# Performance work log

Measured on AMD Instinct MI355X. Metric: run time of the kernel, lower is better.

## Reference

```python
import jax, jax.numpy as jnp
import numpy as np

D_MODEL = 1024
N_HEADS = 16
D_K = D_MODEL // N_HEADS


def setup_inputs() -> dict:
    key = jax.random.key(0)
    k1, k2, k3 = jax.random.split(key, 3)
    x = jax.random.normal(k1, (4, 2048, D_MODEL), dtype=jnp.float32)
    # torch nn.Linear(d, 3d, bias=False): y = x @ W.T ; we store W.T directly as (in, out)
    w_qkv = jax.random.normal(k2, (D_MODEL, 3 * D_MODEL), dtype=jnp.float32) * (1.0 / np.sqrt(D_MODEL))
    w_out = jax.random.normal(k3, (D_MODEL, D_MODEL), dtype=jnp.float32) * (1.0 / np.sqrt(D_MODEL))
    return {"x": x, "w_qkv": w_qkv, "w_out": w_out}


def reference(x, w_qkv, w_out):
    B, T, D = x.shape
    qkv = jnp.einsum('btd,de->bte', x, w_qkv)  # (B,T,3D)
    q, k, v = jnp.split(qkv, 3, axis=-1)
    # split heads -> (B,H,T,d_k)
    def split_heads(t):
        return t.reshape(B, T, N_HEADS, D_K).transpose(0, 2, 1, 3)
    q, k, v = split_heads(q), split_heads(k), split_heads(v)
    scale = 1.0 / np.sqrt(D_K).astype(np.float32)
    scores = jnp.einsum('bhqd,bhkd->bhqk', q, k) * scale  # (B,H,T,T)
    causal = jnp.triu(jnp.full((T, T), -jnp.inf, dtype=scores.dtype), k=1)
    scores = scores + causal[None, None]
    weights = jax.nn.softmax(scores, axis=-1)
    attn = jnp.einsum('bhqk,bhkd->bhqd', weights, v)
    attn = attn.transpose(0, 2, 1, 3).reshape(B, T, D)
    return jnp.einsum('btd,de->bte', attn, w_out)
```

## Files before the change

kernel.cpp:

```cpp
#include <hip/hip_runtime.h>
#include <hip/hip_bf16.h>

typedef short short8 __attribute__((ext_vector_type(8)));
typedef float f32x4 __attribute__((ext_vector_type(4)));

#define MFMA16(a, b, c) __builtin_amdgcn_mfma_f32_16x16x32_bf16((a), (b), (c), 0, 0, 0)

#define GLOAD16(gp, lp)                                                    \
    __builtin_amdgcn_global_load_lds(                                      \
        (const __attribute__((address_space(1))) unsigned int*)(gp),       \
        (__attribute__((address_space(3))) unsigned int*)(lp), 16, 0, 0)

__device__ __forceinline__ unsigned short f2b(float x) {
    unsigned int u = __float_as_uint(x);
    unsigned int r = u + 0x7FFFu + ((u >> 16) & 1u);
    return (unsigned short)(r >> 16);
}

#if __has_builtin(__builtin_amdgcn_cvt_pk_bf16_f32)
__device__ __forceinline__ unsigned pack2(float a, float b) {
    auto v = __builtin_amdgcn_cvt_pk_bf16_f32(a, b);
    unsigned u;
    __builtin_memcpy(&u, &v, 4);
    return u;
}
#else
__device__ __forceinline__ unsigned pack2(float a, float b) {
    return (unsigned)f2b(a) | ((unsigned)f2b(b) << 16);
}
#endif

__global__ __launch_bounds__(256) void cast4_kernel(const float* __restrict__ in,
                                                    unsigned short* __restrict__ out,
                                                    int n4) {
    int i = blockIdx.x * 256 + threadIdx.x;
    if (i < n4) {
        float4 v = ((const float4*)in)[i];
        ushort4 o;
        o.x = f2b(v.x); o.y = f2b(v.y); o.z = f2b(v.z); o.w = f2b(v.w);
        ((ushort4*)out)[i] = o;
    }
}

__global__ __launch_bounds__(256) void transpose_cast_f32(const float* __restrict__ in,
                                                          unsigned short* __restrict__ out,
                                                          int K, int N) {
    __shared__ unsigned short Ls[64 * 66];
    const int k0 = blockIdx.y * 64, n0 = blockIdx.x * 64;
    const int tid = threadIdx.x;
    const int krow = tid >> 4, nc4 = (tid & 15) * 4;
#pragma unroll
    for (int p = 0; p < 4; p++) {
        float4 v = *(const float4*)(in + (size_t)(k0 + krow + p * 16) * N + n0 + nc4);
        unsigned* d32 = (unsigned*)(Ls + (krow + p * 16) * 66 + nc4);
        d32[0] = pack2(v.x, v.y);
        d32[1] = pack2(v.z, v.w);
    }
    __syncthreads();
    const int n = tid >> 3, kc = (tid & 7) * 8;
#pragma unroll
    for (int p = 0; p < 2; p++) {
        int nn = n + p * 32;
        unsigned short w[8];
#pragma unroll
        for (int j = 0; j < 8; j++) w[j] = Ls[(kc + j) * 66 + nn];
        *(short8*)(out + (size_t)(n0 + nn) * K + k0 + kc) = *(short8*)w;
    }
}

__global__ __launch_bounds__(256) void vt_transpose(const unsigned short* __restrict__ qkv,
                                                    unsigned short* __restrict__ Vt) {
    const int T = 2048, E = 3072;
    __shared__ unsigned short Ls[64 * 66];
    const int b = blockIdx.z, h = blockIdx.y, t0 = blockIdx.x * 64;
    const int tid = threadIdx.x;
    const int trow = tid >> 3, dc = (tid & 7) * 8;
    const unsigned short* src = qkv + (size_t)(b * T + t0) * E + 2048 + h * 64;
#pragma unroll
    for (int p = 0; p < 2; p++) {
        short8 v = *(const short8*)(src + (size_t)(trow + p * 32) * E + dc);
        unsigned tmp[4];
        *(short8*)tmp = v;
        unsigned* d32 = (unsigned*)(Ls + (trow + p * 32) * 66 + dc);
        d32[0] = tmp[0]; d32[1] = tmp[1]; d32[2] = tmp[2]; d32[3] = tmp[3];
    }
    __syncthreads();
    const int d = tid >> 3, tc = (tid & 7) * 8;
    const size_t obase = ((size_t)(b * 16 + h) * 64) * 2048;
#pragma unroll
    for (int p = 0; p < 2; p++) {
        int dd = d + p * 32;
        unsigned short w[8];
#pragma unroll
        for (int j = 0; j < 8; j++) w[j] = Ls[(tc + j) * 66 + dd];
        *(short8*)(Vt + obase + (size_t)dd * 2048 + t0 + tc) = *(short8*)w;
    }
}

template <int MT, bool WRITE_BF16, bool SCALE_Q>
__global__ __launch_bounds__(256) void gemm_nt(const unsigned short* __restrict__ A,
                                               const unsigned short* __restrict__ Bt,
                                               void* __restrict__ C,
                                               int M, int N, int K, int lda) {
    constexpr int MI  = MT / 32;
    constexpr int ACH = MT / 64;
    __shared__ unsigned short As[MT * 32];
    __shared__ unsigned short Bs[128 * 32];

    const int tid  = threadIdx.x;
    const int wave = tid >> 6;
    const int lane = tid & 63;
    const int l16  = lane & 15;
    const int quad = lane >> 4;
    const int m0 = blockIdx.y * MT;
    const int n0 = blockIdx.x * 128;
    const int wm = (wave >> 1) * (MT / 2);
    const int wn = (wave & 1) * 64;

    const int srow = lane >> 2;
    const int scol = (((lane & 3) ^ ((lane >> 3) & 3)) * 8);
    const int sw8  = ((l16 >> 1) & 3) * 8;

    const unsigned short* Ag[ACH]; unsigned short* Al[ACH];
#pragma unroll
    for (int p = 0; p < ACH; p++) {
        Ag[p] = A + (size_t)(m0 + (wave * ACH + p) * 16 + srow) * lda + scol;
        Al[p] = As + (wave * ACH + p) * 512;
    }
    const unsigned short* Bg[2]; unsigned short* Bl[2];
#pragma unroll
    for (int p = 0; p < 2; p++) {
        Bg[p] = Bt + (size_t)(n0 + (wave * 2 + p) * 16 + srow) * K + scol;
        Bl[p] = Bs + (wave * 2 + p) * 512;
    }

    f32x4 acc[MI][4] = {};

    for (int k0 = 0; k0 < K; k0 += 32) {
        __syncthreads();
#pragma unroll
        for (int p = 0; p < ACH; p++) GLOAD16(Ag[p] + k0, Al[p]);
#pragma unroll
        for (int p = 0; p < 2; p++) GLOAD16(Bg[p] + k0, Bl[p]);
        __syncthreads();

        short8 af[MI], bf[4];
#pragma unroll
        for (int i = 0; i < MI; i++)
            af[i] = *(const short8*)(As + (wm + i * 16 + l16) * 32 + (quad * 8 ^ sw8));
#pragma unroll
        for (int j = 0; j < 4; j++)
            bf[j] = *(const short8*)(Bs + (wn + j * 16 + l16) * 32 + (quad * 8 ^ sw8));
#pragma unroll
        for (int i = 0; i < MI; i++)
#pragma unroll
            for (int j = 0; j < 4; j++)
                acc[i][j] = MFMA16(af[i], bf[j], acc[i][j]);
    }

    const float QSCALE = 0.125f * 1.44269504f;
#pragma unroll
    for (int i = 0; i < MI; i++)
#pragma unroll
        for (int j = 0; j < 4; j++)
#pragma unroll
            for (int r = 0; r < 4; r++) {
                int row = m0 + wm + i * 16 + quad * 4 + r;
                int col = n0 + wn + j * 16 + l16;
                float v = acc[i][j][r];
                if (SCALE_Q && col < 1024) v *= QSCALE;
                if (WRITE_BF16)
                    ((unsigned short*)C)[(size_t)row * N + col] = f2b(v);
                else
                    ((float*)C)[(size_t)row * N + col] = v;
            }
}

__global__ __launch_bounds__(256) void attention_kernel(const unsigned short* qkv,
                                                        const unsigned short* Vt,
                                                        unsigned short* attn) {
    const int T = 2048, E = 3072;
    const int bi = blockIdx.x;
    const int qb = 31 - (bi >> 6);
    const int hb = bi & 63;
    const int b = hb >> 4, h = hb & 15;
    const int qb0 = qb * 64;
    const int tid = threadIdx.x, wave = tid >> 6, lane = tid & 63;
    const int l16 = lane & 15, quad = lane >> 4;
    const int qw0 = qb0 + wave * 16;

    const unsigned short* Qp  = qkv + (size_t)b * T * E + h * 64;
    const unsigned short* Kp  = Qp + 1024;
    const unsigned short* Vbh = Vt + ((size_t)(b * 16 + h) * 64) * 2048;

    __shared__ unsigned short Ks[2][64 * 32];
    __shared__ unsigned short Vts[2][64 * 32];
    __shared__ unsigned short Ps[4][16 * 40];
    unsigned short* Psw = Ps[wave];

    short8 qf[2];
#pragma unroll
    for (int kd = 0; kd < 2; kd++)
        qf[kd] = *(const short8*)(Qp + (size_t)(qw0 + l16) * E + kd * 32 + quad * 8);

    f32x4 o[4] = {};
    float l_acc = 0.f;

    const int srow = lane >> 2;
    const int scol = (((lane & 3) ^ ((lane >> 3) & 3)) * 8);
    const int sw8  = ((l16 >> 1) & 3) * 8;
    const size_t ktstep = (wave < 2) ? (size_t)64 * E : (size_t)64;
    const size_t cstep  = (wave < 2) ? (size_t)16 * E : (size_t)16 * T;
    const unsigned short* g0 = (wave < 2)
            ? Kp + (size_t)srow * E + wave * 32 + scol
            : Vbh + (size_t)srow * T + (wave - 2) * 32 + scol;
    unsigned short* l0 = (wave < 2) ? Ks[wave] : Vts[wave - 2];

    for (int kt = 0; kt <= qb; kt++) {
        const int tk0 = kt * 64;
        const unsigned short* g = g0 + (size_t)kt * ktstep;
        __syncthreads();
#pragma unroll
        for (int c = 0; c < 4; c++) GLOAD16(g + c * cstep, l0 + c * 512);
        __syncthreads();

#pragma unroll
        for (int th = 0; th < 2; th++) {
            if (tk0 + th * 32 > qw0 + 15) continue;

            f32x4 s[2];
            bool act[2];
#pragma unroll
            for (int mi = 0; mi < 2; mi++) {
                const int t0 = tk0 + (th * 2 + mi) * 16;
                act[mi] = (t0 <= qw0 + 15);
                s[mi] = (f32x4){0.f, 0.f, 0.f, 0.f};
                if (act[mi]) {
                    const int row = (th * 2 + mi) * 16 + l16;
                    short8 kf0 = *(const short8*)(Ks[0] + row * 32 + (quad * 8 ^ sw8));
                    short8 kf1 = *(const short8*)(Ks[1] + row * 32 + (quad * 8 ^ sw8));
                    s[mi] = MFMA16(kf0, qf[0], s[mi]);
                    s[mi] = MFMA16(kf1, qf[1], s[mi]);
                }
            }
#pragma unroll
            for (int mi = 0; mi < 2; mi++) {
                const int t0 = tk0 + (th * 2 + mi) * 16;
                unsigned pk0 = 0, pk1 = 0;
                if (act[mi]) {
                    const bool full = (t0 + 15) <= qw0;
                    float p[4];
#pragma unroll
                    for (int r = 0; r < 4; r++) {
                        float e = __builtin_amdgcn_exp2f(s[mi][r]);
                        if (!full)
                            e = (t0 + quad * 4 + r <= qw0 + l16) ? e : 0.f;
                        p[r] = e;
                    }
                    l_acc += (p[0] + p[1]) + (p[2] + p[3]);
                    pk0 = pack2(p[0], p[1]);
                    pk1 = pack2(p[2], p[3]);
                }
                uint2 pr; pr.x = pk0; pr.y = pk1;
                *(uint2*)(Psw + l16 * 40 + mi * 16 + quad * 4) = pr;
            }
            short8 pf = *(const short8*)(Psw + l16 * 40 + quad * 8);
#pragma unroll
            for (int dt = 0; dt < 4; dt++) {
                short8 vf = *(const short8*)(Vts[th] + (dt * 16 + l16) * 32 + (quad * 8 ^ sw8));
                o[dt] = MFMA16(vf, pf, o[dt]);
            }
        }
    }

    float l = l_acc;
    l += __shfl_xor(l, 16);
    l += __shfl_xor(l, 32);
    const float rl = 1.f / l;
    const int q = qw0 + l16;
#pragma unroll
    for (int dt = 0; dt < 4; dt++) {
        ushort4 wv;
        wv.x = f2b(o[dt][0] * rl);
        wv.y = f2b(o[dt][1] * rl);
        wv.z = f2b(o[dt][2] * rl);
        wv.w = f2b(o[dt][3] * rl);
        *(ushort4*)(attn + (size_t)(b * T + q) * E + h * 64 + dt * 16 + quad * 4) = wv;
    }
}

extern "C" void kernel_launch(void* const* d_in, const int* in_sizes, int n_in,
                              void* d_out, int out_size, void* d_ws, size_t ws_size,
                              hipStream_t stream) {
    const float* x     = (const float*)d_in[0];
    const float* w_qkv = (const float*)d_in[1];
    const float* w_out = (const float*)d_in[2];
    float* out = (float*)d_out;

    const int M = 8192, D = 1024, E = 3072;

    char* ws = (char*)d_ws;
    unsigned short* xb    = (unsigned short*)ws;
    unsigned short* wqkvT = (unsigned short*)(ws + (size_t)16777216);
    unsigned short* woutT = (unsigned short*)(ws + (size_t)23068672);
    unsigned short* qkvb  = (unsigned short*)(ws + (size_t)25165824);
    unsigned short* Vt    = xb;

    cast4_kernel<<<M * D / 4 / 256, 256, 0, stream>>>(x, xb, M * D / 4);
    transpose_cast_f32<<<dim3(E / 64, D / 64), 256, 0, stream>>>(w_qkv, wqkvT, D, E);
    transpose_cast_f32<<<dim3(D / 64, D / 64), 256, 0, stream>>>(w_out, woutT, D, D);

    gemm_nt<128, true, true><<<dim3(E / 128, M / 128), 256, 0, stream>>>(xb, wqkvT, qkvb, M, E, D, D);

    vt_transpose<<<dim3(32, 16, 4), 256, 0, stream>>>(qkvb, Vt);

    attention_kernel<<<dim3(2048), 256, 0, stream>>>(qkvb, Vt, qkvb + 2048);

    gemm_nt<64, false, false><<<dim3(D / 128, M / 64), 256, 0, stream>>>(qkvb + 2048, woutT, out, M, D, D, E);
}
```

Measured before the change: 283.3 us.

## Fuse V transpose into QKV GEMM epilogue and switch GEMMs to 32x32 MFMA

The QKV projection GEMM now writes Q, K and a transposed V directly into separate buffers, staging the V tile through shared memory. This removes the standalone vt_transpose kernel and its extra read and write of V. Both GEMMs move from 16x16x32 to 32x32x16 bf16 MFMA tiles, which need fewer LDS fragment reads per MFMA. Attention writes its output over the Q buffer in place, and the output GEMM reads that buffer with stride 1024. The cost is a more complex epilogue with extra barriers in the V blocks.

```diff
diff --git a/kernel.cpp b/kernel.cpp
--- a/kernel.cpp
+++ b/kernel.cpp
@@ -3,8 +3,10 @@
 
 typedef short short8 __attribute__((ext_vector_type(8)));
 typedef float f32x4 __attribute__((ext_vector_type(4)));
+typedef float f32x16 __attribute__((ext_vector_type(16)));
 
 #define MFMA16(a, b, c) __builtin_amdgcn_mfma_f32_16x16x32_bf16((a), (b), (c), 0, 0, 0)
+#define MFMA32(a, b, c) __builtin_amdgcn_mfma_f32_32x32x16_bf16((a), (b), (c), 0, 0, 0)
 
 #define GLOAD16(gp, lp)                                                    \
     __builtin_amdgcn_global_load_lds(                                      \
@@ -68,118 +70,199 @@
     }
 }
 
-__global__ __launch_bounds__(256) void vt_transpose(const unsigned short* __restrict__ qkv,
-                                                    unsigned short* __restrict__ Vt) {
-    const int T = 2048, E = 3072;
-    __shared__ unsigned short Ls[64 * 66];
-    const int b = blockIdx.z, h = blockIdx.y, t0 = blockIdx.x * 64;
-    const int tid = threadIdx.x;
-    const int trow = tid >> 3, dc = (tid & 7) * 8;
-    const unsigned short* src = qkv + (size_t)(b * T + t0) * E + 2048 + h * 64;
-#pragma unroll
-    for (int p = 0; p < 2; p++) {
-        short8 v = *(const short8*)(src + (size_t)(trow + p * 32) * E + dc);
-        unsigned tmp[4];
-        *(short8*)tmp = v;
-        unsigned* d32 = (unsigned*)(Ls + (trow + p * 32) * 66 + dc);
-        d32[0] = tmp[0]; d32[1] = tmp[1]; d32[2] = tmp[2]; d32[3] = tmp[3];
-    }
-    __syncthreads();
-    const int d = tid >> 3, tc = (tid & 7) * 8;
-    const size_t obase = ((size_t)(b * 16 + h) * 64) * 2048;
-#pragma unroll
-    for (int p = 0; p < 2; p++) {
-        int dd = d + p * 32;
-        unsigned short w[8];
-#pragma unroll
-        for (int j = 0; j < 8; j++) w[j] = Ls[(tc + j) * 66 + dd];
-        *(short8*)(Vt + obase + (size_t)dd * 2048 + t0 + tc) = *(short8*)w;
-    }
-}
-
-template <int MT, bool WRITE_BF16, bool SCALE_Q>
-__global__ __launch_bounds__(256) void gemm_nt(const unsigned short* __restrict__ A,
-                                               const unsigned short* __restrict__ Bt,
-                                               void* __restrict__ C,
-                                               int M, int N, int K, int lda) {
-    constexpr int MI  = MT / 32;
-    constexpr int ACH = MT / 64;
-    __shared__ unsigned short As[MT * 32];
-    __shared__ unsigned short Bs[128 * 32];
+__global__ __launch_bounds__(256) void gemm_qkv(const unsigned short* __restrict__ A,
+                                                const unsigned short* __restrict__ Bt,
+                                                unsigned short* __restrict__ Qb,
+                                                unsigned short* __restrict__ Kb,
+                                                unsigned short* __restrict__ Vt) {
+    const int K = 1024, lda = 1024;
+    __shared__ unsigned short smem[8192];
+    unsigned short* As = smem;
+    unsigned short* Bs = smem + 4096;
 
     const int tid  = threadIdx.x;
     const int wave = tid >> 6;
     const int lane = tid & 63;
-    const int l16  = lane & 15;
-    const int quad = lane >> 4;
-    const int m0 = blockIdx.y * MT;
+    const int l32  = lane & 31;
+    const int hi   = lane >> 5;
+    const int m0 = blockIdx.y * 128;
     const int n0 = blockIdx.x * 128;
-    const int wm = (wave >> 1) * (MT / 2);
+    const int wm = (wave >> 1) * 64;
     const int wn = (wave & 1) * 64;
 
     const int srow = lane >> 2;
     const int scol = (((lane & 3) ^ ((lane >> 3) & 3)) * 8);
-    const int sw8  = ((l16 >> 1) & 3) * 8;
-
-    const unsigned short* Ag[ACH]; unsigned short* Al[ACH];
-#pragma unroll
-    for (int p = 0; p < ACH; p++) {
-        Ag[p] = A + (size_t)(m0 + (wave * ACH + p) * 16 + srow) * lda + scol;
-        Al[p] = As + (wave * ACH + p) * 512;
-    }
-    const unsigned short* Bg[2]; unsigned short* Bl[2];
-#pragma unroll
-    for (int p = 0; p < 2; p++) {
-        Bg[p] = Bt + (size_t)(n0 + (wave * 2 + p) * 16 + srow) * K + scol;
-        Bl[p] = Bs + (wave * 2 + p) * 512;
-    }
-
-    f32x4 acc[MI][4] = {};
+    const int fsw  = ((l32 >> 1) & 3);
+
+    const unsigned short* Ag0 = A  + (size_t)(m0 + wave * 32 + srow)      * lda + scol;
+    const unsigned short* Ag1 = A  + (size_t)(m0 + wave * 32 + 16 + srow) * lda + scol;
+    const unsigned short* Bg0 = Bt + (size_t)(n0 + wave * 32 + srow)      * K + scol;
+    const unsigned short* Bg1 = Bt + (size_t)(n0 + wave * 32 + 16 + srow) * K + scol;
+    unsigned short* Al0 = As + (wave * 2 + 0) * 512;
+    unsigned short* Al1 = As + (wave * 2 + 1) * 512;
+    unsigned short* Bl0 = Bs + (wave * 2 + 0) * 512;
+    unsigned short* Bl1 = Bs + (wave * 2 + 1) * 512;
+
+    f32x16 acc[2][2] = {};
 
     for (int k0 = 0; k0 < K; k0 += 32) {
         __syncthreads();
-#pragma unroll
-        for (int p = 0; p < ACH; p++) GLOAD16(Ag[p] + k0, Al[p]);
-#pragma unroll
-        for (int p = 0; p < 2; p++) GLOAD16(Bg[p] + k0, Bl[p]);
-        __syncthreads();
-
-        short8 af[MI], bf[4];
-#pragma unroll
-        for (int i = 0; i < MI; i++)
-            af[i] = *(const short8*)(As + (wm + i * 16 + l16) * 32 + (quad * 8 ^ sw8));
-#pragma unroll
-        for (int j = 0; j < 4; j++)
-            bf[j] = *(const short8*)(Bs + (wn + j * 16 + l16) * 32 + (quad * 8 ^ sw8));
-#pragma unroll
-        for (int i = 0; i < MI; i++)
-#pragma unroll
-            for (int j = 0; j < 4; j++)
-                acc[i][j] = MFMA16(af[i], bf[j], acc[i][j]);
-    }
-
-    const float QSCALE = 0.125f * 1.44269504f;
-#pragma unroll
-    for (int i = 0; i < MI; i++)
-#pragma unroll
-        for (int j = 0; j < 4; j++)
-#pragma unroll
-            for (int r = 0; r < 4; r++) {
-                int row = m0 + wm + i * 16 + quad * 4 + r;
-                int col = n0 + wn + j * 16 + l16;
-                float v = acc[i][j][r];
-                if (SCALE_Q && col < 1024) v *= QSCALE;
-                if (WRITE_BF16)
-                    ((unsigned short*)C)[(size_t)row * N + col] = f2b(v);
-                else
-                    ((float*)C)[(size_t)row * N + col] = v;
+        GLOAD16(Ag0 + k0, Al0);
+        GLOAD16(Ag1 + k0, Al1);
+        GLOAD16(Bg0 + k0, Bl0);
+        GLOAD16(Bg1 + k0, Bl1);
+        __syncthreads();
+
+        short8 af[2][2], bf[2][2];
+#pragma unroll
+        for (int i = 0; i < 2; i++) {
+            const int row = wm + i * 32 + l32;
+#pragma unroll
+            for (int ks = 0; ks < 2; ks++)
+                af[i][ks] = *(const short8*)(As + row * 32 + ((ks * 2 + hi) ^ fsw) * 8);
+        }
+#pragma unroll
+        for (int j = 0; j < 2; j++) {
+            const int row = wn + j * 32 + l32;
+#pragma unroll
+            for (int ks = 0; ks < 2; ks++)
+                bf[j][ks] = *(const short8*)(Bs + row * 32 + ((ks * 2 + hi) ^ fsw) * 8);
+        }
+#pragma unroll
+        for (int ks = 0; ks < 2; ks++)
+#pragma unroll
+            for (int i = 0; i < 2; i++)
+#pragma unroll
+                for (int j = 0; j < 2; j++)
+                    acc[i][j] = MFMA32(af[i][ks], bf[j][ks], acc[i][j]);
+    }
+
+    if (n0 < 2048) {
+        unsigned short* outp = (n0 < 1024) ? Qb : Kb;
+        const int cb = (n0 < 1024) ? n0 : n0 - 1024;
+        const float QS = (n0 < 1024) ? 0.125f * 1.44269504f : 1.0f;
+#pragma unroll
+        for (int i = 0; i < 2; i++)
+#pragma unroll
+            for (int j = 0; j < 2; j++)
+#pragma unroll
+                for (int r = 0; r < 16; r++) {
+                    int row = m0 + wm + i * 32 + (r & 3) + 8 * (r >> 2) + 4 * hi;
+                    int col = cb + wn + j * 32 + l32;
+                    outp[(size_t)row * 1024 + col] = f2b(acc[i][j][r] * QS);
+                }
+    } else {
+        const int b = m0 >> 11;
+        const int t0b = m0 & 2047;
+        const int hbase = (n0 - 2048) >> 6;
+        __syncthreads();
+#pragma unroll
+        for (int p = 0; p < 2; p++) {
+            if ((wave & 1) == p) {
+#pragma unroll
+                for (int i = 0; i < 2; i++)
+#pragma unroll
+                    for (int j = 0; j < 2; j++) {
+                        const int c = j * 32 + l32;
+#pragma unroll
+                        for (int rg = 0; rg < 4; rg++) {
+                            const int rowbase = wm + i * 32 + rg * 8 + 4 * hi;
+                            uint2 v;
+                            v.x = pack2(acc[i][j][4 * rg + 0], acc[i][j][4 * rg + 1]);
+                            v.y = pack2(acc[i][j][4 * rg + 2], acc[i][j][4 * rg + 3]);
+                            const int w = c * 64 + ((rowbase >> 1) ^ (4 * (c & 7)));
+                            *(uint2*)(smem + 2 * w) = v;
+                        }
+                    }
             }
-}
-
-__global__ __launch_bounds__(256) void attention_kernel(const unsigned short* qkv,
+            __syncthreads();
+#pragma unroll
+            for (int it = 0; it < 4; it++) {
+                const int id = it * 256 + tid;
+                const int c = id >> 4, rg = id & 15;
+                const int w = c * 64 + ((rg * 4) ^ (4 * (c & 7)));
+                short8 v = *(const short8*)(smem + 2 * w);
+                const int h = hbase + p;
+                *(short8*)(Vt + ((size_t)((b * 16 + h) * 64 + c)) * 2048 + t0b + rg * 8) = v;
+            }
+            __syncthreads();
+        }
+    }
+}
+
+__global__ __launch_bounds__(256) void gemm_out(const unsigned short* __restrict__ A,
+                                                const unsigned short* __restrict__ Bt,
+                                                float* __restrict__ C) {
+    const int K = 1024, lda = 1024;
+    __shared__ unsigned short As[64 * 32];
+    __shared__ unsigned short Bs[128 * 32];
+
+    const int tid  = threadIdx.x;
+    const int wave = tid >> 6;
+    const int lane = tid & 63;
+    const int l32  = lane & 31;
+    const int hi   = lane >> 5;
+    const int m0 = blockIdx.y * 64;
+    const int n0 = blockIdx.x * 128;
+    const int wm = (wave >> 1) * 32;
+    const int wn = (wave & 1) * 64;
+
+    const int srow = lane >> 2;
+    const int scol = (((lane & 3) ^ ((lane >> 3) & 3)) * 8);
+    const int fsw  = ((l32 >> 1) & 3);
+
+    const unsigned short* Ag  = A  + (size_t)(m0 + wave * 16 + srow) * lda + scol;
+    const unsigned short* Bg0 = Bt + (size_t)(n0 + wave * 32 + srow)      * K + scol;
+    const unsigned short* Bg1 = Bt + (size_t)(n0 + wave * 32 + 16 + srow) * K + scol;
+    unsigned short* Al  = As + wave * 512;
+    unsigned short* Bl0 = Bs + (wave * 2 + 0) * 512;
+    unsigned short* Bl1 = Bs + (wave * 2 + 1) * 512;
+
+    f32x16 acc[2] = {};
+
+    for (int k0 = 0; k0 < K; k0 += 32) {
+        __syncthreads();
+        GLOAD16(Ag + k0, Al);
+        GLOAD16(Bg0 + k0, Bl0);
+        GLOAD16(Bg1 + k0, Bl1);
+        __syncthreads();
+
+        short8 af[2], bf[2][2];
+        {
+            const int row = wm + l32;
+#pragma unroll
+            for (int ks = 0; ks < 2; ks++)
+                af[ks] = *(const short8*)(As + row * 32 + ((ks * 2 + hi) ^ fsw) * 8);
+        }
+#pragma unroll
+        for (int j = 0; j < 2; j++) {
+            const int row = wn + j * 32 + l32;
+#pragma unroll
+            for (int ks = 0; ks < 2; ks++)
+                bf[j][ks] = *(const short8*)(Bs + row * 32 + ((ks * 2 + hi) ^ fsw) * 8);
+        }
+#pragma unroll
+        for (int ks = 0; ks < 2; ks++)
+#pragma unroll
+            for (int j = 0; j < 2; j++)
+                acc[j] = MFMA32(af[ks], bf[j][ks], acc[j]);
+    }
+
+#pragma unroll
+    for (int j = 0; j < 2; j++)
+#pragma unroll
+        for (int r = 0; r < 16; r++) {
+            int row = m0 + wm + (r & 3) + 8 * (r >> 2) + 4 * hi;
+            int col = n0 + wn + j * 32 + l32;
+            C[(size_t)row * 1024 + col] = acc[j][r];
+        }
+}
+
+__global__ __launch_bounds__(256) void attention_kernel(const unsigned short* Qb,
+                                                        const unsigned short* Kb,
                                                         const unsigned short* Vt,
                                                         unsigned short* attn) {
-    const int T = 2048, E = 3072;
+    const int T = 2048;
     const int bi = blockIdx.x;
     const int qb = 31 - (bi >> 6);
     const int hb = bi & 63;
@@ -189,8 +272,8 @@
     const int l16 = lane & 15, quad = lane >> 4;
     const int qw0 = qb0 + wave * 16;
 
-    const unsigned short* Qp  = qkv + (size_t)b * T * E + h * 64;
-    const unsigned short* Kp  = Qp + 1024;
+    const unsigned short* Qp  = Qb + (size_t)b * T * 1024 + h * 64;
+    const unsigned short* Kp  = Kb + (size_t)b * T * 1024 + h * 64;
     const unsigned short* Vbh = Vt + ((size_t)(b * 16 + h) * 64) * 2048;
 
     __shared__ unsigned short Ks[2][64 * 32];
@@ -201,7 +284,7 @@
     short8 qf[2];
 #pragma unroll
     for (int kd = 0; kd < 2; kd++)
-        qf[kd] = *(const short8*)(Qp + (size_t)(qw0 + l16) * E + kd * 32 + quad * 8);
+        qf[kd] = *(const short8*)(Qp + (size_t)(qw0 + l16) * 1024 + kd * 32 + quad * 8);
 
     f32x4 o[4] = {};
     float l_acc = 0.f;
@@ -209,10 +292,10 @@
     const int srow = lane >> 2;
     const int scol = (((lane & 3) ^ ((lane >> 3) & 3)) * 8);
     const int sw8  = ((l16 >> 1) & 3) * 8;
-    const size_t ktstep = (wave < 2) ? (size_t)64 * E : (size_t)64;
-    const size_t cstep  = (wave < 2) ? (size_t)16 * E : (size_t)16 * T;
+    const size_t ktstep = (wave < 2) ? (size_t)64 * 1024 : (size_t)64;
+    const size_t cstep  = (wave < 2) ? (size_t)16 * 1024 : (size_t)16 * T;
     const unsigned short* g0 = (wave < 2)
-            ? Kp + (size_t)srow * E + wave * 32 + scol
+            ? Kp + (size_t)srow * 1024 + wave * 32 + scol
             : Vbh + (size_t)srow * T + (wave - 2) * 32 + scol;
     unsigned short* l0 = (wave < 2) ? Ks[wave] : Vts[wave - 2];
 
@@ -285,7 +368,7 @@
         wv.y = f2b(o[dt][1] * rl);
         wv.z = f2b(o[dt][2] * rl);
         wv.w = f2b(o[dt][3] * rl);
-        *(ushort4*)(attn + (size_t)(b * T + q) * E + h * 64 + dt * 16 + quad * 4) = wv;
+        *(ushort4*)(attn + (size_t)(b * T + q) * 1024 + h * 64 + dt * 16 + quad * 4) = wv;
     }
 }
 
@@ -298,23 +381,23 @@
     float* out = (float*)d_out;
 
     const int M = 8192, D = 1024, E = 3072;
+    const size_t MB = 1048576;
 
     char* ws = (char*)d_ws;
     unsigned short* xb    = (unsigned short*)ws;
-    unsigned short* wqkvT = (unsigned short*)(ws + (size_t)16777216);
-    unsigned short* woutT = (unsigned short*)(ws + (size_t)23068672);
-    unsigned short* qkvb  = (unsigned short*)(ws + (size_t)25165824);
-    unsigned short* Vt    = xb;
+    unsigned short* wqkvT = (unsigned short*)(ws + 16 * MB);
+    unsigned short* woutT = (unsigned short*)(ws + 22 * MB);
+    unsigned short* Qb    = (unsigned short*)(ws + 24 * MB);
+    unsigned short* Kb    = (unsigned short*)(ws + 40 * MB);
+    unsigned short* Vt    = (unsigned short*)(ws + 56 * MB);
 
     cast4_kernel<<<M * D / 4 / 256, 256, 0, stream>>>(x, xb, M * D / 4);
     transpose_cast_f32<<<dim3(E / 64, D / 64), 256, 0, stream>>>(w_qkv, wqkvT, D, E);
     transpose_cast_f32<<<dim3(D / 64, D / 64), 256, 0, stream>>>(w_out, woutT, D, D);
 
-    gemm_nt<128, true, true><<<dim3(E / 128, M / 128), 256, 0, stream>>>(xb, wqkvT, qkvb, M, E, D, D);
-
-    vt_transpose<<<dim3(32, 16, 4), 256, 0, stream>>>(qkvb, Vt);
-
-    attention_kernel<<<dim3(2048), 256, 0, stream>>>(qkvb, Vt, qkvb + 2048);
-
-    gemm_nt<64, false, false><<<dim3(D / 128, M / 64), 256, 0, stream>>>(qkvb + 2048, woutT, out, M, D, D, E);
-}
+    gemm_qkv<<<dim3(E / 128, M / 128), 256, 0, stream>>>(xb, wqkvT, Qb, Kb, Vt);
+
+    attention_kernel<<<dim3(2048), 256, 0, stream>>>(Qb, Kb, Vt, Qb);
+
+    gemm_out<<<dim3(D / 128, M / 64), 256, 0, stream>>>(Qb, woutT, out);
+}
```

Result: faster. 268.8 us (-5.1%).
